# Kernel tuning notes

Hardware: AMD Instinct MI355X
Metric: run time of the kernel (lower is better)

## Reference

```python
import jax, jax.numpy as jnp
import numpy as np

# IR-Net EDE surrogate-gradient constants (ir_1w1a.IRConv2d defaults)
K = 10.0
T = 0.1
BN_EPS = 1e-5

@jax.custom_vjp
def binary_quantize(x):
    return jnp.sign(x)

def _bq_fwd(x):
    return jnp.sign(x), x

def _bq_bwd(x, g):
    # grad = k * t * (1 - tanh(x*t)^2) * g   (IR-Net BinaryQuantize.backward)
    return (K * T * (1.0 - jnp.tanh(x * T) ** 2) * g,)

binary_quantize.defvjp(_bq_fwd, _bq_bwd)


def setup_inputs() -> dict:
    key = jax.random.key(0)
    k1, k2 = jax.random.split(key, 2)
    return {
        "x": jax.random.normal(k1, (32, 256, 56, 56), dtype=jnp.float32),
        "weight": jax.random.normal(k2, (256, 256, 3, 3), dtype=jnp.float32) * 0.05,
        "gamma": jnp.ones((256,), dtype=jnp.float32),
        "beta": jnp.zeros((256,), dtype=jnp.float32),
    }


def _convalg(x, weight, gamma, beta):
    co = weight.shape[0]
    wf = weight.reshape(co, -1)
    # per-output-channel standardization of weights
    bw = weight - wf.mean(-1).reshape(co, 1, 1, 1)
    std = jnp.std(bw.reshape(co, -1), axis=-1, ddof=1).reshape(co, 1, 1, 1)  # torch unbiased std
    bw = bw / std
    # detached power-of-2 per-channel scale: sw = 2^round(log2(mean|bw|))
    sw = jax.lax.stop_gradient(
        2.0 ** jnp.round(jnp.log2(jnp.abs(bw).reshape(co, -1).mean(-1)))
    ).reshape(co, 1, 1, 1)
    bwq = binary_quantize(bw) * sw   # binarized, scaled weights {-sw, +sw}
    ba = binary_quantize(x)          # binarized activations {-1, +1}
    y = jax.lax.conv_general_dilated(
        ba, bwq,
        window_strides=(1, 1),
        padding=((1, 1), (1, 1)),
        dimension_numbers=("NCHW", "OIHW", "NCHW"),
    )
    # BatchNorm2d, training-mode forward (batch statistics, biased variance)
    mean = y.mean(axis=(0, 2, 3), keepdims=True)
    var = y.var(axis=(0, 2, 3), keepdims=True)
    yn = (y - mean) * jax.lax.rsqrt(var + BN_EPS)
    yn = yn * gamma.reshape(1, -1, 1, 1) + beta.reshape(1, -1, 1, 1)
    # Hardtanh
    return jnp.clip(yn, -1.0, 1.0)


def reference(x, weight, gamma, beta):
    return _convalg(x, weight, gamma, beta)
```

## Files before the change

### kernel.cpp

```cpp
#include <hip/hip_runtime.h>
#include <math.h>

#define HH 56
#define WW 56
#define NB 32
#define CC 256
#define PIX 3136
#define M_TOT 100352
#define PADH 58
#define PADW 58
#define ACTQ_BYTES ((size_t)NB*PADH*PADW*CC)
#define WQ_BYTES ((size_t)9*CC*CC)
#define SBUF_BYTES ((size_t)M_TOT*CC*2)
#define BM 128
#define BN 128

typedef unsigned int u32;
typedef unsigned long long u64;
typedef int v4i __attribute__((ext_vector_type(4)));

typedef const __attribute__((address_space(1))) unsigned int* as1_u32p;
typedef __attribute__((address_space(3))) unsigned int* as3_u32p;
#define GLOAD_LDS16(g, l) \
  __builtin_amdgcn_global_load_lds((as1_u32p)(g), (as3_u32p)(l), 16, 0, 0)

__global__ __launch_bounds__(256) void pack_weights_i8(
    const float* __restrict__ wt, signed char* __restrict__ wq,
    float* __restrict__ swv,
    long long* __restrict__ sumS, long long* __restrict__ sumSS) {
  int co = blockIdx.x;
  int t  = threadIdx.x;
  int lane = t & 63, wid = t >> 6;

  float wv[9];
  const float* wp = wt + ((size_t)co*CC + t)*9;
  double psum = 0.0;
#pragma unroll
  for (int k = 0; k < 9; ++k) { wv[k] = wp[k]; psum += (double)wv[k]; }

  __shared__ double redm[4];
#pragma unroll
  for (int off = 32; off > 0; off >>= 1) psum += __shfl_xor(psum, off);
  if (lane == 0) redm[wid] = psum;
  __syncthreads();
  double mean = (redm[0]+redm[1]+redm[2]+redm[3]) * (1.0/2304.0);

  double pabs = 0.0, psq = 0.0;
#pragma unroll
  for (int k = 0; k < 9; ++k) {
    double d = (double)wv[k] - mean;
    pabs += fabs(d);
    psq  += d*d;
  }
#pragma unroll
  for (int off = 32; off > 0; off >>= 1) {
    pabs += __shfl_xor(pabs, off);
    psq  += __shfl_xor(psq,  off);
  }
  __shared__ double reda[4], redq[4];
  if (lane == 0) { reda[wid] = pabs; redq[wid] = psq; }
  __syncthreads();
  if (t == 0) {
    double sa = reda[0]+reda[1]+reda[2]+reda[3];
    double sq = redq[0]+redq[1]+redq[2]+redq[3];
    double stdv = sqrt(sq / 2303.0);
    double mabs = (sa * (1.0/2304.0)) / stdv;
    swv[co] = (float)exp2(rint(log2(mabs)));
    sumS[co]  = 0;
    sumSS[co] = 0;
  }
#pragma unroll
  for (int k = 0; k < 9; ++k)
    wq[((size_t)k*CC + co)*CC + t] =
        (((double)wv[k] - mean) > 0.0) ? (signed char)1 : (signed char)-1;
}

__global__ __launch_bounds__(256) void pack_acts_i8(
    const float* __restrict__ x, signed char* __restrict__ actq) {
  int n = blockIdx.y, tile = blockIdx.x;
  int lane = threadIdx.x & 63, cw = threadIdx.x >> 6;
  int pp = tile*64 + lane;
  if (pp >= PADH*PADW) return;
  int ph = pp / PADW, pw = pp - ph*PADW;
  signed char* dst = actq + ((size_t)(n*PADH + ph)*PADW + pw)*CC + cw*64;
  if (ph == 0 || ph == PADH-1 || pw == 0 || pw == PADW-1) {
    uint4 z = make_uint4(0u, 0u, 0u, 0u);
#pragma unroll
    for (int q = 0; q < 4; ++q) ((uint4*)dst)[q] = z;
    return;
  }
  int h = ph - 1, w = pw - 1;
  const float* xp = x + ((size_t)(n*CC + cw*64))*PIX + h*WW + w;
  u32 wrd[16];
#pragma unroll
  for (int c16 = 0; c16 < 16; ++c16) {
    u32 v = 0;
#pragma unroll
    for (int b = 0; b < 4; ++b) {
      float f = xp[(size_t)(c16*4 + b)*PIX];
      v |= (f > 0.0f ? 0x01u : 0xFFu) << (8*b);
    }
    wrd[c16] = v;
  }
#pragma unroll
  for (int q = 0; q < 4; ++q)
    ((uint4*)dst)[q] = make_uint4(wrd[4*q], wrd[4*q+1], wrd[4*q+2], wrd[4*q+3]);
}

template <bool S16>
__global__ __launch_bounds__(256, 3) void bconv_mfma(
    const signed char* __restrict__ actq, const signed char* __restrict__ wq,
    short* __restrict__ s16out, float* __restrict__ f32out,
    u64* __restrict__ sumS, u64* __restrict__ sumSS) {
  __shared__ char lds[32768] __attribute__((aligned(16)));
  __shared__ int colS[128], colQ[128];

  int t = threadIdx.x;
  int lane = t & 63, wv = t >> 6;
  int lm = lane & 15, quad = lane >> 4;
  int ar0 = (wv & 1) * 64;
  int bc0 = (wv >> 1) * 64;
  int Mbase = blockIdx.x * BM;
  int n0 = blockIdx.y * BN;

  if (t < 128) { colS[t] = 0; colQ[t] = 0; }

  int r = t >> 2, c16 = t & 3;
  const signed char *pA0, *pA1;
  {
    int P = Mbase + r;
    int n_ = P / PIX, pl_ = P % PIX, h_ = pl_ / WW, w_ = pl_ % WW;
    pA0 = actq + ((size_t)(n_*PADH + h_+1)*PADW + (w_+1))*CC + c16*16;
    P += 64;
    n_ = P / PIX; pl_ = P % PIX; h_ = pl_ / WW; w_ = pl_ % WW;
    pA1 = actq + ((size_t)(n_*PADH + h_+1)*PADW + (w_+1))*CC + c16*16;
  }
  const signed char* pB0 = wq + (size_t)(n0 + r)*CC + c16*16;
  const signed char* pB1 = pB0 + 64*CC;
  int ldst = t*16;

  v4i acc[4][4];
#pragma unroll
  for (int i = 0; i < 4; ++i)
#pragma unroll
    for (int j = 0; j < 4; ++j) acc[i][j] = 0;

  {
    int aoff = (-PADW - 1)*CC;
    GLOAD_LDS16(pA0 + aoff, lds + ldst);
    GLOAD_LDS16(pA1 + aoff, lds + 4096 + ldst);
    GLOAD_LDS16(pB0, lds + 8192 + ldst);
    GLOAD_LDS16(pB1, lds + 12288 + ldst);
  }

#pragma unroll 1
  for (int s = 0; s < 36; ++s) {
    __syncthreads();
    if (s < 35) {
      int sn = s + 1;
      int tn = sn >> 2, kn = sn & 3;
      int aoff = ((tn/3 - 1)*PADW + (tn%3 - 1))*CC + kn*64;
      int boff = tn*65536 + kn*64;
      char* nb = (char*)lds + ((sn & 1) << 14);
      GLOAD_LDS16(pA0 + aoff, nb + ldst);
      GLOAD_LDS16(pA1 + aoff, nb + 4096 + ldst);
      GLOAD_LDS16(pB0 + boff, nb + 8192 + ldst);
      GLOAD_LDS16(pB1 + boff, nb + 12288 + ldst);
    }
    const char* cb = (const char*)lds + ((s & 1) << 14);
    v4i af[4], bf[4];
#pragma unroll
    for (int i = 0; i < 4; ++i)
      af[i] = *(const v4i*)(cb + (ar0 + i*16 + lm)*64 + quad*16);
#pragma unroll
    for (int j = 0; j < 4; ++j)
      bf[j] = *(const v4i*)(cb + 8192 + (bc0 + j*16 + lm)*64 + quad*16);
#pragma unroll
    for (int i = 0; i < 4; ++i)
#pragma unroll
      for (int j = 0; j < 4; ++j)
        acc[i][j] = __builtin_amdgcn_mfma_i32_16x16x64_i8(af[i], bf[j],
                                                          acc[i][j], 0, 0, 0);
  }

  int Sl[4] = {0,0,0,0}, Ql[4] = {0,0,0,0};
#pragma unroll
  for (int i = 0; i < 4; ++i) {
    int R = Mbase + ar0 + i*16 + quad*4;
    int nR = R / PIX, plR = R % PIX;
#pragma unroll
    for (int j = 0; j < 4; ++j) {
      int colo = n0 + bc0 + j*16 + lm;
      v4i a = acc[i][j];
      size_t idx = ((size_t)nR*CC + colo)*PIX + plR;
      if (S16) {
        int2 pk;
        pk.x = (a.x & 0xFFFF) | (a.y << 16);
        pk.y = (a.z & 0xFFFF) | (a.w << 16);
        *(int2*)(s16out + idx) = pk;
      } else {
        *(float4*)(f32out + idx) =
            make_float4((float)a.x, (float)a.y, (float)a.z, (float)a.w);
      }
      Sl[j] += a.x + a.y + a.z + a.w;
      Ql[j] += a.x*a.x + a.y*a.y + a.z*a.z + a.w*a.w;
    }
  }
#pragma unroll
  for (int j = 0; j < 4; ++j) {
    int S = Sl[j], Q = Ql[j];
    S += __shfl_xor(S, 16); S += __shfl_xor(S, 32);
    Q += __shfl_xor(Q, 16); Q += __shfl_xor(Q, 32);
    if (quad == 0) {
      atomicAdd(&colS[bc0 + j*16 + lm], S);
      atomicAdd(&colQ[bc0 + j*16 + lm], Q);
    }
  }
  __syncthreads();
  if (t < 128) {
    atomicAdd(&sumS[n0 + t], (u64)(long long)colS[t]);
    atomicAdd(&sumSS[n0 + t], (u64)(long long)colQ[t]);
  }
}

__global__ void finalize_stats(
    const long long* __restrict__ sumS, const long long* __restrict__ sumSS,
    const float* __restrict__ swv,
    const float* __restrict__ gamma, const float* __restrict__ beta,
    float* __restrict__ AB) {
  int c = threadIdx.x;
  double mu  = (double)sumS[c]  / (double)M_TOT;
  double var = (double)sumSS[c] / (double)M_TOT - mu*mu;
  double sw  = (double)swv[c];
  double inv = 1.0 / sqrt(sw*sw*var + 1e-5);
  double scale = (double)gamma[c] * sw * inv;
  double shift = (double)beta[c] - scale * mu;
  AB[c]      = (float)scale;
  AB[CC + c] = (float)shift;
}

__global__ __launch_bounds__(256) void bn_apply_s16(
    const short* __restrict__ s, float* __restrict__ out,
    const float* __restrict__ AB, int n8) {
  int i = blockIdx.x*256 + threadIdx.x;
  if (i >= n8) return;
  union { int4 v; short sh[8]; } u;
  u.v = ((const int4*)s)[i];
  int c = ((i*8) / PIX) & (CC-1);
  float a = AB[c], b = AB[CC + c];
  float4 o0, o1;
  o0.x = fminf(1.f, fmaxf(-1.f, (float)u.sh[0]*a + b));
  o0.y = fminf(1.f, fmaxf(-1.f, (float)u.sh[1]*a + b));
  o0.z = fminf(1.f, fmaxf(-1.f, (float)u.sh[2]*a + b));
  o0.w = fminf(1.f, fmaxf(-1.f, (float)u.sh[3]*a + b));
  o1.x = fminf(1.f, fmaxf(-1.f, (float)u.sh[4]*a + b));
  o1.y = fminf(1.f, fmaxf(-1.f, (float)u.sh[5]*a + b));
  o1.z = fminf(1.f, fmaxf(-1.f, (float)u.sh[6]*a + b));
  o1.w = fminf(1.f, fmaxf(-1.f, (float)u.sh[7]*a + b));
  ((float4*)out)[2*i]   = o0;
  ((float4*)out)[2*i+1] = o1;
}

__global__ __launch_bounds__(256) void bn_apply_f32(
    float* __restrict__ out, const float* __restrict__ AB, int n4) {
  int i = blockIdx.x*256 + threadIdx.x;
  if (i >= n4) return;
  float4 v = ((float4*)out)[i];
  int c = ((i*4) / PIX) & (CC-1);
  float a = AB[c], b = AB[CC + c];
  v.x = fminf(1.f, fmaxf(-1.f, v.x*a + b));
  v.y = fminf(1.f, fmaxf(-1.f, v.y*a + b));
  v.z = fminf(1.f, fmaxf(-1.f, v.z*a + b));
  v.w = fminf(1.f, fmaxf(-1.f, v.w*a + b));
  ((float4*)out)[i] = v;
}

extern "C" void kernel_launch(void* const* d_in, const int* in_sizes, int n_in,
                              void* d_out, int out_size, void* d_ws, size_t ws_size,
                              hipStream_t stream) {
  (void)in_sizes; (void)n_in; (void)out_size;
  const float* x     = (const float*)d_in[0];
  const float* wt    = (const float*)d_in[1];
  const float* gamma = (const float*)d_in[2];
  const float* beta  = (const float*)d_in[3];
  float* out = (float*)d_out;

  char* ws = (char*)d_ws;
  size_t off = 0;
  signed char* actq = (signed char*)(ws + off);
  off += ACTQ_BYTES;             off = (off + 255) & ~(size_t)255;
  signed char* wq = (signed char*)(ws + off);
  off += WQ_BYTES;               off = (off + 255) & ~(size_t)255;
  float* swv = (float*)(ws + off); off += 1024;
  float* AB  = (float*)(ws + off); off += 2048;
  long long* sumS  = (long long*)(ws + off); off += 2048;
  long long* sumSS = (long long*)(ws + off); off += 2048;
  off = (off + 255) & ~(size_t)255;
  short* sbuf = (short*)(ws + off);
  bool s16 = (ws_size >= off + SBUF_BYTES);

  pack_weights_i8<<<256, 256, 0, stream>>>(wt, wq, swv, sumS, sumSS);
  pack_acts_i8<<<dim3(53, NB), 256, 0, stream>>>(x, actq);
  if (s16) {
    bconv_mfma<true><<<dim3(M_TOT/BM, CC/BN), 256, 0, stream>>>(
        actq, wq, sbuf, nullptr, (u64*)sumS, (u64*)sumSS);
  } else {
    bconv_mfma<false><<<dim3(M_TOT/BM, CC/BN), 256, 0, stream>>>(
        actq, wq, nullptr, out, (u64*)sumS, (u64*)sumSS);
  }
  finalize_stats<<<1, 256, 0, stream>>>(sumS, sumSS, swv, gamma, beta, AB);
  if (s16) {
    bn_apply_s16<<<(M_TOT*CC/8 + 255)/256, 256, 0, stream>>>(
        sbuf, out, AB, M_TOT*CC/8);
  } else {
    bn_apply_f32<<<(M_TOT*CC/4 + 255)/256, 256, 0, stream>>>(
        out, AB, M_TOT*CC/4);
  }
}
```

Measured before the change: 163.9 us.

## Triple-buffer int8 MFMA conv mainloop with swizzled LDS and explicit waitcnts

The double-buffered LDS loop with a full syncthreads per step becomes a three-stage pipeline. Loads are issued three steps ahead, and explicit vmcnt waits and barriers replace the implicit full drain. It adds an XOR swizzle on the 16-byte chunk index for both global-to-LDS writes and fragment reads to reduce LDS bank conflicts, and raises wave priority around the MFMA block. LDS use grows from 32KB to 48KB per block, which may reduce occupancy below the 3-blocks launch bound.

```diff
diff --git a/kernel.cpp b/kernel.cpp
--- a/kernel.cpp
+++ b/kernel.cpp
@@ -107,12 +107,48 @@
     ((uint4*)dst)[q] = make_uint4(wrd[4*q], wrd[4*q+1], wrd[4*q+2], wrd[4*q+3]);
 }
 
+
+#define STAGEM(SN, BUF) do {                                              \
+    int tn_ = (SN) >> 2, kn_ = (SN) & 3;                                  \
+    int aoff_ = ((tn_/3 - 1)*PADW + (tn_%3 - 1))*CC + kn_*64;             \
+    int boff_ = tn_*65536 + kn_*64;                                       \
+    char* nb_ = (char*)lds + (BUF)*16384;                                 \
+    GLOAD_LDS16(pA0 + aoff_, nb_ + ldst);                                 \
+    GLOAD_LDS16(pA1 + aoff_, nb_ + 4096 + ldst);                          \
+    GLOAD_LDS16(pB0 + boff_, nb_ + 8192 + ldst);                          \
+    GLOAD_LDS16(pB1 + boff_, nb_ + 12288 + ldst);                         \
+  } while (0)
+
+#define STEPM(S, BUF, WTXT, DOSTAGE) do {                                 \
+    asm volatile("s_waitcnt " WTXT ::: "memory");                         \
+    __builtin_amdgcn_s_barrier();                                         \
+    const char* cb_ = (const char*)lds + (BUF)*16384;                     \
+    v4i af[4], bf[4];                                                     \
+    _Pragma("unroll")                                                     \
+    for (int i = 0; i < 4; ++i)                                           \
+      af[i] = *(const v4i*)(cb_ + (ar0 + i*16 + lm)*64 + rdo);            \
+    _Pragma("unroll")                                                     \
+    for (int j = 0; j < 4; ++j)                                           \
+      bf[j] = *(const v4i*)(cb_ + 8192 + (bc0 + j*16 + lm)*64 + rdo);     \
+    asm volatile("s_waitcnt lgkmcnt(0)" ::: "memory");                    \
+    __builtin_amdgcn_s_barrier();                                         \
+    if (DOSTAGE) { STAGEM((S) + 3, BUF); }                                \
+    __builtin_amdgcn_s_setprio(1);                                        \
+    _Pragma("unroll")                                                     \
+    for (int i = 0; i < 4; ++i)                                           \
+      _Pragma("unroll")                                                   \
+      for (int j = 0; j < 4; ++j)                                         \
+        acc[i][j] = __builtin_amdgcn_mfma_i32_16x16x64_i8(af[i], bf[j],   \
+                                                          acc[i][j], 0, 0, 0); \
+    __builtin_amdgcn_s_setprio(0);                                        \
+  } while (0)
+
 template <bool S16>
 __global__ __launch_bounds__(256, 3) void bconv_mfma(
     const signed char* __restrict__ actq, const signed char* __restrict__ wq,
     short* __restrict__ s16out, float* __restrict__ f32out,
     u64* __restrict__ sumS, u64* __restrict__ sumSS) {
-  __shared__ char lds[32768] __attribute__((aligned(16)));
+  __shared__ char lds[49152] __attribute__((aligned(16)));
   __shared__ int colS[128], colQ[128];
 
   int t = threadIdx.x;
@@ -126,62 +162,41 @@
   if (t < 128) { colS[t] = 0; colQ[t] = 0; }
 
   int r = t >> 2, c16 = t & 3;
+  int cs = c16 ^ ((r >> 1) & 3);
   const signed char *pA0, *pA1;
   {
     int P = Mbase + r;
     int n_ = P / PIX, pl_ = P % PIX, h_ = pl_ / WW, w_ = pl_ % WW;
-    pA0 = actq + ((size_t)(n_*PADH + h_+1)*PADW + (w_+1))*CC + c16*16;
+    pA0 = actq + ((size_t)(n_*PADH + h_+1)*PADW + (w_+1))*CC + cs*16;
     P += 64;
     n_ = P / PIX; pl_ = P % PIX; h_ = pl_ / WW; w_ = pl_ % WW;
-    pA1 = actq + ((size_t)(n_*PADH + h_+1)*PADW + (w_+1))*CC + c16*16;
-  }
-  const signed char* pB0 = wq + (size_t)(n0 + r)*CC + c16*16;
+    pA1 = actq + ((size_t)(n_*PADH + h_+1)*PADW + (w_+1))*CC + cs*16;
+  }
+  const signed char* pB0 = wq + (size_t)(n0 + r)*CC + cs*16;
   const signed char* pB1 = pB0 + 64*CC;
   int ldst = t*16;
 
+  int rdo = (quad ^ ((lm >> 1) & 3)) * 16;
+
   v4i acc[4][4];
 #pragma unroll
   for (int i = 0; i < 4; ++i)
 #pragma unroll
     for (int j = 0; j < 4; ++j) acc[i][j] = 0;
 
-  {
-    int aoff = (-PADW - 1)*CC;
-    GLOAD_LDS16(pA0 + aoff, lds + ldst);
-    GLOAD_LDS16(pA1 + aoff, lds + 4096 + ldst);
-    GLOAD_LDS16(pB0, lds + 8192 + ldst);
-    GLOAD_LDS16(pB1, lds + 12288 + ldst);
-  }
+  STAGEM(0, 0);
+  STAGEM(1, 1);
+  STAGEM(2, 2);
 
 #pragma unroll 1
-  for (int s = 0; s < 36; ++s) {
-    __syncthreads();
-    if (s < 35) {
-      int sn = s + 1;
-      int tn = sn >> 2, kn = sn & 3;
-      int aoff = ((tn/3 - 1)*PADW + (tn%3 - 1))*CC + kn*64;
-      int boff = tn*65536 + kn*64;
-      char* nb = (char*)lds + ((sn & 1) << 14);
-      GLOAD_LDS16(pA0 + aoff, nb + ldst);
-      GLOAD_LDS16(pA1 + aoff, nb + 4096 + ldst);
-      GLOAD_LDS16(pB0 + boff, nb + 8192 + ldst);
-      GLOAD_LDS16(pB1 + boff, nb + 12288 + ldst);
-    }
-    const char* cb = (const char*)lds + ((s & 1) << 14);
-    v4i af[4], bf[4];
-#pragma unroll
-    for (int i = 0; i < 4; ++i)
-      af[i] = *(const v4i*)(cb + (ar0 + i*16 + lm)*64 + quad*16);
-#pragma unroll
-    for (int j = 0; j < 4; ++j)
-      bf[j] = *(const v4i*)(cb + 8192 + (bc0 + j*16 + lm)*64 + quad*16);
-#pragma unroll
-    for (int i = 0; i < 4; ++i)
-#pragma unroll
-      for (int j = 0; j < 4; ++j)
-        acc[i][j] = __builtin_amdgcn_mfma_i32_16x16x64_i8(af[i], bf[j],
-                                                          acc[i][j], 0, 0, 0);
-  }
+  for (int s = 0; s < 33; s += 3) {
+    STEPM(s,     0, "vmcnt(8)", true);
+    STEPM(s + 1, 1, "vmcnt(8)", true);
+    STEPM(s + 2, 2, "vmcnt(8)", true);
+  }
+  STEPM(33, 0, "vmcnt(8)", false);
+  STEPM(34, 1, "vmcnt(4)", false);
+  STEPM(35, 2, "vmcnt(0)", false);
 
   int Sl[4] = {0,0,0,0}, Ql[4] = {0,0,0,0};
 #pragma unroll
```

After: 162.0 us. No clear change (-1.2%).
